# Performance work log

Measured on AMD Instinct MI355X. Metric: run time of the kernel, lower is better.

## Reference

```python
import jax, jax.numpy as jnp
import numpy as np

G, NODES, H, E = 64, 511, 768, 4096
N = NODES + 1  # +1 graph token


def setup_inputs() -> dict:
    key = jax.random.key(0)
    ks = jax.random.split(key, 7)
    node_emb = jax.random.normal(ks[0], (4, H), dtype=jnp.float32) * 0.02
    node_emb = node_emb.at[0].set(0.0)  # padding_idx=0
    graph_emb = jax.random.normal(ks[1], (1, H), dtype=jnp.float32) * 0.02
    W_l = jax.random.normal(ks[2], (H, H), dtype=jnp.float32) / np.sqrt(H)
    b_l = jnp.zeros((H,), dtype=jnp.float32)
    W_r = jax.random.normal(ks[3], (H, H), dtype=jnp.float32) / np.sqrt(H)
    input_nodes = jax.random.randint(ks[4], (G, NODES), 0, 4, dtype=jnp.int64) if jax.config.jax_enable_x64 else jax.random.randint(ks[4], (G, NODES), 0, 4, dtype=jnp.int32)
    input_edges = jax.random.randint(ks[5], (G, 2, E), 0, N, dtype=jnp.int32)
    return {"input_nodes": input_nodes, "input_edges": input_edges,
            "node_emb": node_emb, "graph_emb": graph_emb,
            "W_l": W_l, "b_l": b_l, "W_r": W_r}


def _sage_conv(x, edges, W_l, b_l, W_r):
    # PyG SAGEConv (mean aggr): out = lin_l(mean_{j in N(i)} x_j) + lin_r(x_i)
    # x: [G, N, H]; edges: [G, 2, E] (row0 = src, row1 = dst)
    g, n, h = x.shape
    src, dst = edges[:, 0, :], edges[:, 1, :]                       # [G, E]
    offs = (jnp.arange(g, dtype=src.dtype) * n)[:, None]
    fs = (src + offs).reshape(-1)                                   # flat src ids
    fd = (dst + offs).reshape(-1)                                   # flat dst ids
    xf = x.reshape(g * n, h)
    msg = xf[fs]                                                    # gather [G*E, H]
    agg = jax.ops.segment_sum(msg, fd, num_segments=g * n)          # scatter-add
    deg = jax.ops.segment_sum(jnp.ones_like(fd, dtype=x.dtype), fd, num_segments=g * n)
    mean = agg / jnp.maximum(deg, 1.0)[:, None]
    out = mean @ W_l.T + b_l + xf @ W_r.T
    return out.reshape(g, n, h)


def reference(input_nodes, input_edges, node_emb, graph_emb, W_l, b_l, W_r):
    g = input_nodes.shape[0]
    node_feature = node_emb[input_nodes]                            # [G, NODES, H]
    graph_token = jnp.broadcast_to(graph_emb[None], (g, 1, node_emb.shape[1]))
    graph_node_feature = jnp.concatenate([graph_token, node_feature], axis=1)  # [G, N, H]
    graph_edge_feature = _sage_conv(graph_node_feature, input_edges, W_l, b_l, W_r)
    return (graph_node_feature, graph_edge_feature)
```

## Files before the change

kernel.cpp:

```cpp
#include <hip/hip_runtime.h>

#define G_     64
#define NODES_ 511
#define NN_    512
#define H_     768
#define E_     4096
#define NTYPE  5

#define PROJB_ 960
#define GNFB_  2048

typedef float f32x4 __attribute__((ext_vector_type(4)));

__global__ __launch_bounds__(512)
void prep_kernel(const int* __restrict__ edges,
                 const int* __restrict__ nodes,
                 const float* __restrict__ node_emb,
                 const float* __restrict__ graph_emb,
                 const float* __restrict__ W_l,
                 const float* __restrict__ b_l,
                 const float* __restrict__ W_r,
                 float* __restrict__ params,
                 float* __restrict__ P_l,
                 float* __restrict__ P_r,
                 float* __restrict__ gnf)
{
    int t = threadIdx.x;
    if (blockIdx.x < G_) {
        __shared__ int hist[NN_ * NTYPE];
        int g = blockIdx.x;

        #pragma unroll
        for (int i = 0; i < NN_ * NTYPE / 512; ++i)
            hist[t + i * 512] = 0;
        __syncthreads();

        const int* eg = edges + (size_t)g * 2 * E_;
        const int* ng = nodes + (size_t)g * NODES_;
        #pragma unroll
        for (int i = 0; i < E_ / 512; ++i) {
            int e = t + i * 512;
            int src = eg[e];
            int dst = eg[E_ + e];
            int type = (src == 0) ? 0 : (ng[src - 1] + 1);
            atomicAdd(&hist[dst * NTYPE + type], 1);
        }
        __syncthreads();

        {
            int n = t;
            float c0 = (float)hist[n * NTYPE + 0];
            float c1 = (float)hist[n * NTYPE + 1];
            float c2 = (float)hist[n * NTYPE + 2];
            float c3 = (float)hist[n * NTYPE + 3];
            float c4 = (float)hist[n * NTYPE + 4];
            float inv = 1.0f / fmaxf(c0 + c1 + c2 + c3 + c4, 1.0f);
            int ty = (n == 0) ? 0 : (ng[n - 1] + 1);
            f32x4 v0 = {c0 * inv, c1 * inv, c2 * inv, c3 * inv};
            f32x4 v1 = {c4 * inv, __int_as_float(ty), 0.0f, 0.0f};
            float* pp = params + ((size_t)g * NN_ + n) * 8;
            *(f32x4*)pp       = v0;
            *(f32x4*)(pp + 4) = v1;
        }
    } else if (blockIdx.x < G_ + PROJB_) {
        int wave = (blockIdx.x - G_) * 8 + (t >> 6);
        int lane = t & 63;
        int m = wave / (NTYPE * H_);
        int r = wave % (NTYPE * H_);
        int ty = r / H_;
        int j = r % H_;
        const float* emb = (ty == 0) ? graph_emb : (node_emb + (size_t)(ty - 1) * H_);
        const float* W   = ((m == 0) ? W_l : W_r) + (size_t)j * H_;

        float a0, a1, a2;
        {
            int k0 = lane * 4;
            f32x4 w0 = *(const f32x4*)(W + k0);
            f32x4 e0 = *(const f32x4*)(emb + k0);
            f32x4 w1 = *(const f32x4*)(W + k0 + 256);
            f32x4 e1 = *(const f32x4*)(emb + k0 + 256);
            f32x4 w2 = *(const f32x4*)(W + k0 + 512);
            f32x4 e2 = *(const f32x4*)(emb + k0 + 512);
            a0 = w0.x * e0.x + w0.y * e0.y + w0.z * e0.z + w0.w * e0.w;
            a1 = w1.x * e1.x + w1.y * e1.y + w1.z * e1.z + w1.w * e1.w;
            a2 = w2.x * e2.x + w2.y * e2.y + w2.z * e2.z + w2.w * e2.w;
        }
        float acc = a0 + a1 + a2;
        #pragma unroll
        for (int off = 32; off; off >>= 1)
            acc += __shfl_xor(acc, off, 64);

        if (lane == 0) {
            if (m == 0) P_l[ty * H_ + j] = acc;
            else        P_r[ty * H_ + j] = acc + b_l[j];
        }
    } else {
        int wv   = (blockIdx.x - (G_ + PROJB_)) * 8 + (t >> 6);
        int lane = t & 63;
        int k0   = lane * 4;
        #pragma unroll
        for (int i = 0; i < 2; ++i) {
            int row = wv * 2 + i;
            int g = row >> 9;
            int n = row & (NN_ - 1);
            int ty = (n == 0) ? 0 : (nodes[g * NODES_ + n - 1] + 1);
            const float* er = (ty == 0) ? graph_emb
                                        : (node_emb + (size_t)(ty - 1) * H_);
            size_t roff = (size_t)row * H_ + k0;
            #pragma unroll
            for (int c = 0; c < 3; ++c) {
                f32x4 ev = *(const f32x4*)(er + k0 + c * 256);
                *(f32x4*)(gnf + roff + c * 256) = ev;
            }
        }
    }
}

__global__ __launch_bounds__(256)
void gef_kernel(const float* __restrict__ params,
                const float* __restrict__ P_l,
                const float* __restrict__ P_r,
                float* __restrict__ gef)
{
    int wave = blockIdx.x * 4 + (threadIdx.x >> 6);
    int lane = threadIdx.x & 63;
    int k0   = lane * 4;

    f32x4 pl[NTYPE][3];
    #pragma unroll
    for (int tt = 0; tt < NTYPE; ++tt) {
        #pragma unroll
        for (int c = 0; c < 3; ++c)
            pl[tt][c] = *(const f32x4*)(P_l + (size_t)tt * H_ + k0 + c * 256);
    }

    int row0 = wave * 4;
    #pragma unroll
    for (int i = 0; i < 4; ++i) {
        int row = row0 + i;
        const float* pp = params + (size_t)row * 8;
        f32x4 v0 = *(const f32x4*)pp;
        f32x4 v1 = *(const f32x4*)(pp + 4);
        int ty = __float_as_int(v1.y);
        const float* prr = P_r + (size_t)ty * H_;
        size_t roff = (size_t)row * H_ + k0;

        #pragma unroll
        for (int c = 0; c < 3; ++c) {
            f32x4 pr = *(const f32x4*)(prr + k0 + c * 256);
            f32x4 o  = v0.x * pl[0][c] + v0.y * pl[1][c] + v0.z * pl[2][c]
                     + v0.w * pl[3][c] + v1.x * pl[4][c] + pr;
            *(f32x4*)(gef + roff + c * 256) = o;
        }
    }
}

extern "C" void kernel_launch(void* const* d_in, const int* in_sizes, int n_in,
                              void* d_out, int out_size, void* d_ws, size_t ws_size,
                              hipStream_t stream)
{
    const int*   input_nodes = (const int*)d_in[0];
    const int*   input_edges = (const int*)d_in[1];
    const float* node_emb    = (const float*)d_in[2];
    const float* graph_emb   = (const float*)d_in[3];
    const float* W_l         = (const float*)d_in[4];
    const float* b_l         = (const float*)d_in[5];
    const float* W_r         = (const float*)d_in[6];

    float* gnf = (float*)d_out;
    float* gef = gnf + (size_t)G_ * NN_ * H_;

    float* params = (float*)d_ws;
    float* P_l = params + (size_t)G_ * NN_ * 8;
    float* P_r = P_l + NTYPE * H_;

    prep_kernel<<<G_ + PROJB_ + GNFB_, 512, 0, stream>>>(
        input_edges, input_nodes, node_emb, graph_emb, W_l, b_l, W_r,
        params, P_l, P_r, gnf);

    gef_kernel<<<(G_ * NN_) / 16, 256, 0, stream>>>(
        params, P_l, P_r, gef);
}
```

Measured before the change: 215.1 us.

## Reuse weight rows across types and register-cache embeddings in gnf/gef writers

The projection blocks now compute all five type dot products per weight row, so W_l/W_r are read once instead of five times, which cuts the projection grid from 960 to 192 blocks. The gnf writer keeps the five embedding column slices in registers and selects per row instead of gathering from a type-dependent pointer. The gef kernel uses one thread per 4-column slice across 16 rows with P_l/P_r held in registers and a select in place of the indexed P_r load. Both writer paths mainly cut redundant loads on a store-bound kernel, at the cost of more registers and a changed block shape.

```diff
diff --git a/kernel.cpp b/kernel.cpp
--- a/kernel.cpp
+++ b/kernel.cpp
@@ -7,8 +7,8 @@
 #define E_     4096
 #define NTYPE  5
 
-#define PROJB_ 960
-#define GNFB_  2048
+#define PROJB_ 192
+#define GNFB_  1536
 
 typedef float f32x4 __attribute__((ext_vector_type(4)));
 
@@ -65,93 +65,111 @@
     } else if (blockIdx.x < G_ + PROJB_) {
         int wave = (blockIdx.x - G_) * 8 + (t >> 6);
         int lane = t & 63;
-        int m = wave / (NTYPE * H_);
-        int r = wave % (NTYPE * H_);
-        int ty = r / H_;
-        int j = r % H_;
-        const float* emb = (ty == 0) ? graph_emb : (node_emb + (size_t)(ty - 1) * H_);
-        const float* W   = ((m == 0) ? W_l : W_r) + (size_t)j * H_;
-
-        float a0, a1, a2;
-        {
-            int k0 = lane * 4;
-            f32x4 w0 = *(const f32x4*)(W + k0);
+        int m = wave / H_;
+        int j = wave % H_;
+
+        const float* W = ((m == 0) ? W_l : W_r) + (size_t)j * H_;
+        int k0 = lane * 4;
+        f32x4 w0 = *(const f32x4*)(W + k0);
+        f32x4 w1 = *(const f32x4*)(W + k0 + 256);
+        f32x4 w2 = *(const f32x4*)(W + k0 + 512);
+
+        float acc[NTYPE];
+        #pragma unroll
+        for (int ty = 0; ty < NTYPE; ++ty) {
+            const float* emb = (ty == 0) ? graph_emb
+                                         : (node_emb + (size_t)(ty - 1) * H_);
             f32x4 e0 = *(const f32x4*)(emb + k0);
-            f32x4 w1 = *(const f32x4*)(W + k0 + 256);
             f32x4 e1 = *(const f32x4*)(emb + k0 + 256);
-            f32x4 w2 = *(const f32x4*)(W + k0 + 512);
             f32x4 e2 = *(const f32x4*)(emb + k0 + 512);
-            a0 = w0.x * e0.x + w0.y * e0.y + w0.z * e0.z + w0.w * e0.w;
-            a1 = w1.x * e1.x + w1.y * e1.y + w1.z * e1.z + w1.w * e1.w;
-            a2 = w2.x * e2.x + w2.y * e2.y + w2.z * e2.z + w2.w * e2.w;
-        }
-        float acc = a0 + a1 + a2;
-        #pragma unroll
-        for (int off = 32; off; off >>= 1)
-            acc += __shfl_xor(acc, off, 64);
+            acc[ty] = w0.x*e0.x + w0.y*e0.y + w0.z*e0.z + w0.w*e0.w
+                    + w1.x*e1.x + w1.y*e1.y + w1.z*e1.z + w1.w*e1.w
+                    + w2.x*e2.x + w2.y*e2.y + w2.z*e2.z + w2.w*e2.w;
+        }
+        #pragma unroll
+        for (int ty = 0; ty < NTYPE; ++ty) {
+            #pragma unroll
+            for (int off = 32; off; off >>= 1)
+                acc[ty] += __shfl_xor(acc[ty], off, 64);
+        }
 
         if (lane == 0) {
-            if (m == 0) P_l[ty * H_ + j] = acc;
-            else        P_r[ty * H_ + j] = acc + b_l[j];
+            if (m == 0) {
+                #pragma unroll
+                for (int ty = 0; ty < NTYPE; ++ty) P_l[ty * H_ + j] = acc[ty];
+            } else {
+                float b = b_l[j];
+                #pragma unroll
+                for (int ty = 0; ty < NTYPE; ++ty) P_r[ty * H_ + j] = acc[ty] + b;
+            }
         }
     } else {
-        int wv   = (blockIdx.x - (G_ + PROJB_)) * 8 + (t >> 6);
+        int W    = (blockIdx.x - (G_ + PROJB_)) * 8 + (t >> 6);
         int lane = t & 63;
-        int k0   = lane * 4;
-        #pragma unroll
-        for (int i = 0; i < 2; ++i) {
-            int row = wv * 2 + i;
+        int c    = W >> 12;
+        int h0   = c * 256 + lane * 4;
+
+        f32x4 em0 = *(const f32x4*)(graph_emb + h0);
+        f32x4 em1 = *(const f32x4*)(node_emb + 0 * H_ + h0);
+        f32x4 em2 = *(const f32x4*)(node_emb + 1 * H_ + h0);
+        f32x4 em3 = *(const f32x4*)(node_emb + 2 * H_ + h0);
+        f32x4 em4 = *(const f32x4*)(node_emb + 3 * H_ + h0);
+
+        int row0 = (W & 4095) * 8;
+        #pragma unroll
+        for (int i = 0; i < 8; ++i) {
+            int row = row0 + i;
             int g = row >> 9;
             int n = row & (NN_ - 1);
             int ty = (n == 0) ? 0 : (nodes[g * NODES_ + n - 1] + 1);
-            const float* er = (ty == 0) ? graph_emb
-                                        : (node_emb + (size_t)(ty - 1) * H_);
-            size_t roff = (size_t)row * H_ + k0;
-            #pragma unroll
-            for (int c = 0; c < 3; ++c) {
-                f32x4 ev = *(const f32x4*)(er + k0 + c * 256);
-                *(f32x4*)(gnf + roff + c * 256) = ev;
-            }
+            f32x4 v = em0;
+            v = (ty == 1) ? em1 : v;
+            v = (ty == 2) ? em2 : v;
+            v = (ty == 3) ? em3 : v;
+            v = (ty == 4) ? em4 : v;
+            *(f32x4*)(gnf + (size_t)row * H_ + h0) = v;
         }
     }
 }
 
-__global__ __launch_bounds__(256)
+__global__ __launch_bounds__(192)
 void gef_kernel(const float* __restrict__ params,
                 const float* __restrict__ P_l,
                 const float* __restrict__ P_r,
                 float* __restrict__ gef)
 {
-    int wave = blockIdx.x * 4 + (threadIdx.x >> 6);
-    int lane = threadIdx.x & 63;
-    int k0   = lane * 4;
-
-    f32x4 pl[NTYPE][3];
-    #pragma unroll
-    for (int tt = 0; tt < NTYPE; ++tt) {
-        #pragma unroll
-        for (int c = 0; c < 3; ++c)
-            pl[tt][c] = *(const f32x4*)(P_l + (size_t)tt * H_ + k0 + c * 256);
-    }
-
-    int row0 = wave * 4;
-    #pragma unroll
-    for (int i = 0; i < 4; ++i) {
+    int tid = threadIdx.x;
+    int h0  = tid * 4;
+
+    f32x4 pl0 = *(const f32x4*)(P_l + 0 * H_ + h0);
+    f32x4 pl1 = *(const f32x4*)(P_l + 1 * H_ + h0);
+    f32x4 pl2 = *(const f32x4*)(P_l + 2 * H_ + h0);
+    f32x4 pl3 = *(const f32x4*)(P_l + 3 * H_ + h0);
+    f32x4 pl4 = *(const f32x4*)(P_l + 4 * H_ + h0);
+    f32x4 pr0 = *(const f32x4*)(P_r + 0 * H_ + h0);
+    f32x4 pr1 = *(const f32x4*)(P_r + 1 * H_ + h0);
+    f32x4 pr2 = *(const f32x4*)(P_r + 2 * H_ + h0);
+    f32x4 pr3 = *(const f32x4*)(P_r + 3 * H_ + h0);
+    f32x4 pr4 = *(const f32x4*)(P_r + 4 * H_ + h0);
+
+    int row0 = blockIdx.x * 16;
+    #pragma unroll 4
+    for (int i = 0; i < 16; ++i) {
         int row = row0 + i;
         const float* pp = params + (size_t)row * 8;
         f32x4 v0 = *(const f32x4*)pp;
         f32x4 v1 = *(const f32x4*)(pp + 4);
         int ty = __float_as_int(v1.y);
-        const float* prr = P_r + (size_t)ty * H_;
-        size_t roff = (size_t)row * H_ + k0;
-
-        #pragma unroll
-        for (int c = 0; c < 3; ++c) {
-            f32x4 pr = *(const f32x4*)(prr + k0 + c * 256);
-            f32x4 o  = v0.x * pl[0][c] + v0.y * pl[1][c] + v0.z * pl[2][c]
-                     + v0.w * pl[3][c] + v1.x * pl[4][c] + pr;
-            *(f32x4*)(gef + roff + c * 256) = o;
-        }
+
+        f32x4 sel = pr0;
+        sel = (ty == 1) ? pr1 : sel;
+        sel = (ty == 2) ? pr2 : sel;
+        sel = (ty == 3) ? pr3 : sel;
+        sel = (ty == 4) ? pr4 : sel;
+
+        f32x4 o = v0.x * pl0 + v0.y * pl1 + v0.z * pl2
+                + v0.w * pl3 + v1.x * pl4 + sel;
+        *(f32x4*)(gef + (size_t)row * H_ + h0) = o;
     }
 }
 
@@ -178,6 +196,6 @@
         input_edges, input_nodes, node_emb, graph_emb, W_l, b_l, W_r,
         params, P_l, P_r, gnf);
 
-    gef_kernel<<<(G_ * NN_) / 16, 256, 0, stream>>>(
+    gef_kernel<<<(G_ * NN_) / 16, 192, 0, stream>>>(
         params, P_l, P_r, gef);
 }
```

Measured after the change: 218.7 us. About the same (+1.7%).
